# Optimization experiments

Measured on AMD Instinct MI355X. Metric: run time of the kernel, lower is better.

The kernel has to match this reference:

```python
import jax, jax.numpy as jnp
import numpy as np

T, N = 128, 2048
D_LIN, D_AC, D_IM = 300, 74, 35
H_LIN, H_AC, H_IM = 88, 48, 88
TOT_H = H_LIN + H_AC + H_IM          # 224
ATT_IN = 2 * TOT_H                   # 448 (window_dim=2)
MEM = 128
GAMMA_IN = ATT_IN + MEM              # 576
FINAL = TOT_H + MEM                  # 352
OUT_DIM = 1


def _lin(x, w, b):
    # torch nn.Linear: y = x @ W^T + b, W: [out, in]
    return x @ w.T + b


def _lstm_cell(x, h, c, w_ih, w_hh, b_ih, b_hh):
    # torch nn.LSTMCell gate order: i, f, g, o
    gates = x @ w_ih.T + b_ih + h @ w_hh.T + b_hh
    i, f, g, o = jnp.split(gates, 4, axis=-1)
    c2 = jax.nn.sigmoid(f) * c + jax.nn.sigmoid(i) * jnp.tanh(g)
    h2 = jax.nn.sigmoid(o) * jnp.tanh(c2)
    return h2, c2


def _forward(x_lin, x_ac, x_im, p):
    (W_ih_lin, W_hh_lin, b_ih_lin, b_hh_lin,
     W_ih_ac, W_hh_ac, b_ih_ac, b_hh_ac,
     W_ih_im, W_hh_im, b_ih_im, b_hh_im,
     att1_w1, att1_b1, att1_w2, att1_b2,
     att2_w1, att2_b1, att2_w2, att2_b2,
     g1_w1, g1_b1, g1_w2, g1_b2,
     g2_w1, g2_b1, g2_w2, g2_b2,
     out_w1, out_b1, out_w2, out_b2) = p
    n = x_lin.shape[1]
    z = lambda d: jnp.zeros((n, d), dtype=x_lin.dtype)
    init = (z(H_LIN), z(H_LIN), z(H_AC), z(H_AC), z(H_IM), z(H_IM), z(MEM))

    def step(carry, xs):
        h_l, c_l, h_a, c_a, h_i, c_i, mem = carry
        xl, xa, xi = xs
        nh_l, nc_l = _lstm_cell(xl, h_l, c_l, W_ih_lin, W_hh_lin, b_ih_lin, b_hh_lin)
        nh_a, nc_a = _lstm_cell(xa, h_a, c_a, W_ih_ac, W_hh_ac, b_ih_ac, b_hh_ac)
        nh_i, nc_i = _lstm_cell(xi, h_i, c_i, W_ih_im, W_hh_im, b_ih_im, b_hh_im)
        prev_cs = jnp.concatenate([c_l, c_a, c_i], axis=1)
        new_cs = jnp.concatenate([nc_l, nc_a, nc_i], axis=1)
        c_star = jnp.concatenate([prev_cs, new_cs], axis=1)   # [n, 448]
        attn = jax.nn.softmax(
            _lin(jax.nn.relu(_lin(c_star, att1_w1, att1_b1)), att1_w2, att1_b2), axis=1)
        attended = attn * c_star
        c_hat = jnp.tanh(
            _lin(jax.nn.relu(_lin(attended, att2_w1, att2_b1)), att2_w2, att2_b2))
        both = jnp.concatenate([attended, mem], axis=1)       # [n, 576]
        gamma1 = jax.nn.sigmoid(_lin(jax.nn.relu(_lin(both, g1_w1, g1_b1)), g1_w2, g1_b2))
        gamma2 = jax.nn.sigmoid(_lin(jax.nn.relu(_lin(both, g2_w1, g2_b1)), g2_w2, g2_b2))
        new_mem = gamma1 * mem + gamma2 * c_hat
        return ((nh_l, nc_l, nh_a, nc_a, nh_i, nc_i, new_mem),
                (nh_l, nh_a, nh_i, new_mem))

    _, (hs_l, hs_a, hs_i, mems) = jax.lax.scan(step, init, (x_lin, x_ac, x_im))
    feats = jnp.concatenate([hs_l, hs_a, hs_i, mems], axis=-1)  # [T, n, 352]
    out = _lin(jax.nn.relu(_lin(feats, out_w1, out_b1)), out_w2, out_b2)  # [T, n, 1]
    return jnp.transpose(out, (1, 0, 2))  # [n, T, 1] (torch cats over dim=1)


def setup_inputs() -> dict:
    key = jax.random.key(0)
    ks = iter(jax.random.split(key, 64))

    def rn(shape, s=0.05):
        return (jax.random.normal(next(ks), shape) * s).astype(jnp.float32)

    inp = {
        'x_linguistic': rn((T, N, D_LIN), 1.0),
        'x_acoustic': rn((T, N, D_AC), 1.0),
        'x_image': rn((T, N, D_IM), 1.0),
    }
    for name, din, h in [('lin', D_LIN, H_LIN), ('ac', D_AC, H_AC), ('im', D_IM, H_IM)]:
        inp[f'W_ih_{name}'] = rn((4 * h, din))
        inp[f'W_hh_{name}'] = rn((4 * h, h))
        inp[f'b_ih_{name}'] = rn((4 * h,))
        inp[f'b_hh_{name}'] = rn((4 * h,))
    for nm, hdim, din, dout in [('att1', 128, ATT_IN, ATT_IN),
                                ('att2', 256, ATT_IN, MEM),
                                ('g1', 64, GAMMA_IN, MEM),
                                ('g2', 64, GAMMA_IN, MEM),
                                ('out', 64, FINAL, OUT_DIM)]:
        inp[f'{nm}_w1'] = rn((hdim, din))
        inp[f'{nm}_b1'] = rn((hdim,))
        inp[f'{nm}_w2'] = rn((dout, hdim))
        inp[f'{nm}_b2'] = rn((dout,))
    return inp


def reference(x_linguistic, x_acoustic, x_image,
              W_ih_lin, W_hh_lin, b_ih_lin, b_hh_lin,
              W_ih_ac, W_hh_ac, b_ih_ac, b_hh_ac,
              W_ih_im, W_hh_im, b_ih_im, b_hh_im,
              att1_w1, att1_b1, att1_w2, att1_b2,
              att2_w1, att2_b1, att2_w2, att2_b2,
              g1_w1, g1_b1, g1_w2, g1_b2,
              g2_w1, g2_b1, g2_w2, g2_b2,
              out_w1, out_b1, out_w2, out_b2):
    p = (W_ih_lin, W_hh_lin, b_ih_lin, b_hh_lin,
         W_ih_ac, W_hh_ac, b_ih_ac, b_hh_ac,
         W_ih_im, W_hh_im, b_ih_im, b_hh_im,
         att1_w1, att1_b1, att1_w2, att1_b2,
         att2_w1, att2_b1, att2_w2, att2_b2,
         g1_w1, g1_b1, g1_w2, g1_b2,
         g2_w1, g2_b1, g2_w2, g2_b2,
         out_w1, out_b1, out_w2, out_b2)
    return _forward(x_linguistic, x_acoustic, x_image, p)
```

## Files before the change

kernel.cpp:

```cpp
#include <hip/hip_runtime.h>


#define T_STEPS 128

typedef __attribute__((ext_vector_type(8))) short bf16x8;
typedef __attribute__((ext_vector_type(4))) float f32x4;
typedef __attribute__((ext_vector_type(2))) unsigned long long ull2;

#define MFMA_B16(a,b,c) __builtin_amdgcn_mfma_f32_16x16x32_bf16((a),(b),(c),0,0,0)

__device__ __forceinline__ unsigned short f2b(float v) {
  union { float f; unsigned u; } x; x.f = v;
  unsigned r = x.u + 0x7fffu + ((x.u >> 16) & 1u);
  return (unsigned short)(r >> 16);
}
__device__ __forceinline__ float b2f(unsigned short u) {
  union { unsigned u; float f; } x; x.u = ((unsigned)u) << 16; return x.f;
}
__device__ __forceinline__ float sigm(float x){ return 1.0f/(1.0f + __expf(-x)); }
__device__ __forceinline__ float tanh_(float x){ return 1.0f - 2.0f/(1.0f + __expf(2.0f*x)); }

#define OFF_XL     0
#define OFF_XA     10496
#define OFF_XI     13824
#define OFF_CSTAR  16128
#define OFF_ATT    30720
#define OFF_HID    45312
#define OFF_G1H    53760
#define OFF_G2H    56064
#define OFF_FEATS  58368
#define OFF_BIAS   69888
#define OFF_XP     79368
#define LDS_BYTES  110344

#define BG_LIN 0
#define BG_AC  384
#define BG_IM  576
#define B_A1H  960
#define B_LOG  1088
#define B_A2H  1536
#define B_CHAT 1792
#define B_G1H  1920
#define B_G2H  1984
#define B_GM1  2048
#define B_GM2  2176
#define B_OUTH 2304
#define B_OUT2 2368
#define N_BIAS 2369

#define N_TILES 1718
#define PACK_BYTES ((size_t)N_TILES * 1024)
#define XP_ELEMS ((size_t)262144 * 960)
#define XP_BYTES (XP_ELEMS * 2)

#define LA(off,st,row,kk)  (*(const bf16x8*)(lds + (off) + ((((row)*(st)) + (kk)) << 1)))
#define LB(tile)           (*(const bf16x8*)(packc + (((size_t)(tile)) << 10) + (lane << 4)))
#define STB(off,st,row,col,v) (*(unsigned short*)(lds + (off) + ((((row)*(st)) + (col)) << 1)) = f2b(v))
#define LDB(off,st,row,col)   b2f(*(const unsigned short*)(lds + (off) + ((((row)*(st)) + (col)) << 1)))

struct PP { const float* p[35]; };

__device__ __forceinline__ void vmw(int n) {
  switch (n) {
    case 0:  asm volatile("s_waitcnt vmcnt(0)");  break;
    case 1:  asm volatile("s_waitcnt vmcnt(1)");  break;
    case 2:  asm volatile("s_waitcnt vmcnt(2)");  break;
    case 3:  asm volatile("s_waitcnt vmcnt(3)");  break;
    case 4:  asm volatile("s_waitcnt vmcnt(4)");  break;
    case 5:  asm volatile("s_waitcnt vmcnt(5)");  break;
    case 6:  asm volatile("s_waitcnt vmcnt(6)");  break;
    case 7:  asm volatile("s_waitcnt vmcnt(7)");  break;
    case 8:  asm volatile("s_waitcnt vmcnt(8)");  break;
    case 9:  asm volatile("s_waitcnt vmcnt(9)");  break;
    case 10: asm volatile("s_waitcnt vmcnt(10)"); break;
    case 11: asm volatile("s_waitcnt vmcnt(11)"); break;
    case 12: asm volatile("s_waitcnt vmcnt(12)"); break;
    case 13: asm volatile("s_waitcnt vmcnt(13)"); break;
    case 14: asm volatile("s_waitcnt vmcnt(14)"); break;
    default: asm volatile("s_waitcnt vmcnt(15)"); break;
  }
  __builtin_amdgcn_sched_barrier(0);
}

#define ISSUE_B(dst, tile)                                                   \
  { unsigned off_ = (((unsigned)(tile)) << 10) + ((unsigned)lane << 4);      \
    asm volatile("global_load_dwordx4 %0, %1, %2"                            \
                 : "=v"(dst) : "v"(off_), "s"(packc)); }

template<int NTT, class FT, class FB>
__device__ __forceinline__ void reg_loop(const char* packc, int lane,
                                         FT&& tile_of, FB&& body)
{
  constexpr int D = (NTT < 16) ? NTT : 16;
  bf16x8 b[16];
  #pragma unroll
  for (int i = 0; i < D; ++i) ISSUE_B(b[i], tile_of(i));
  #pragma unroll
  for (int i = 0; i < NTT; ++i) {
    vmw((NTT-1-i) < 15 ? (NTT-1-i) : 15);
    body(i, b[i & 15]);
    __builtin_amdgcn_sched_barrier(0);
    if (i + 16 < NTT) ISSUE_B(b[i & 15], tile_of(i + 16));
  }
}

__device__ __forceinline__ float gate_src(const float* Wih, const float* Whh,
                                          int H, int din, int nksx, int col, int k)
{
  int blk = col >> 6, gate = (col >> 4) & 3, u = col & 15;
  int unit = blk*16 + u;
  if (unit >= H) return 0.f;
  int row = gate*H + unit;
  int xk = nksx*32;
  if (k < xk) return (k < din) ? Wih[row*din + k] : 0.f;
  int kk = k - xk;
  return (kk < H) ? Whh[row*H + kk] : 0.f;
}
__device__ __forceinline__ float gate_h(const float* Whh, int H, int col, int k)
{
  int blk = col >> 6, gate = (col >> 4) & 3, u = col & 15;
  int unit = blk*16 + u;
  if (unit >= H || k >= H) return 0.f;
  return Whh[(gate*H + unit)*H + k];
}
__device__ __forceinline__ float gate_x(const float* Wih, int H, int din, int col, int k)
{
  int blk = col >> 6, gate = (col >> 4) & 3, u = col & 15;
  int unit = blk*16 + u;
  if (unit >= H || k >= din) return 0.f;
  return Wih[(gate*H + unit)*din + k];
}
__device__ __forceinline__ float plain_src(const float* W, int nout, int kdim, int col, int k)
{
  return (col < nout && k < kdim) ? W[col*kdim + k] : 0.f;
}

__global__ __launch_bounds__(256) void pack_kernel(PP P, unsigned short* __restrict__ pack,
                                                   float* __restrict__ bias)
{
  int tid = blockIdx.x*blockDim.x + threadIdx.x;
  int wv = tid >> 6, lane = tid & 63;
  int nw = (gridDim.x*blockDim.x) >> 6;
  int c = lane & 15, kg = lane >> 4;

  for (int tile = wv; tile < N_TILES; tile += nw) {
    unsigned short* dst = pack + ((size_t)tile << 9) + lane*8;
    #pragma unroll
    for (int i = 0; i < 8; ++i) {
      int r = tile; int nt, ks; float v; int kk;
      if (r < 312)       { nt=r/13; ks=r-nt*13; kk=ks*32+kg*8+i; v = gate_src(P.p[3], P.p[4], 88,300,10, nt*16+c, kk); }
      else if (r < 372)  { r-=312; nt=r/5;  ks=r-nt*5;  kk=ks*32+kg*8+i; v = gate_src(P.p[7], P.p[8], 48, 74, 3, nt*16+c, kk); }
      else if (r < 492)  { r-=372; nt=r/5;  ks=r-nt*5;  kk=ks*32+kg*8+i; v = gate_src(P.p[11],P.p[12],88, 35, 2, nt*16+c, kk); }
      else if (r < 604)  { r-=492; nt=r/14; ks=r-nt*14; kk=ks*32+kg*8+i; v = plain_src(P.p[15],128,448, nt*16+c, kk); }
      else if (r < 716)  { r-=604; nt=r/4;  ks=r-nt*4;  kk=ks*32+kg*8+i; v = plain_src(P.p[17],448,128, nt*16+c, kk); }
      else if (r < 940)  { r-=716; nt=r/14; ks=r-nt*14; kk=ks*32+kg*8+i; v = plain_src(P.p[19],256,448, nt*16+c, kk); }
      else if (r < 1004) { r-=940; nt=r/8;  ks=r-nt*8;  kk=ks*32+kg*8+i; v = plain_src(P.p[21],128,256, nt*16+c, kk); }
      else if (r < 1076) { r-=1004; nt=r/18; ks=r-nt*18; kk=ks*32+kg*8+i; v = plain_src(P.p[23], 64,576, nt*16+c, kk); }
      else if (r < 1148) { r-=1076; nt=r/18; ks=r-nt*18; kk=ks*32+kg*8+i; v = plain_src(P.p[27], 64,576, nt*16+c, kk); }
      else if (r < 1164) { r-=1148; nt=r/2;  ks=r-nt*2;  kk=ks*32+kg*8+i; v = plain_src(P.p[25],128, 64, nt*16+c, kk); }
      else if (r < 1180) { r-=1164; nt=r/2;  ks=r-nt*2;  kk=ks*32+kg*8+i; v = plain_src(P.p[29],128, 64, nt*16+c, kk); }
      else if (r < 1224) { r-=1180; nt=r/11; ks=r-nt*11; kk=ks*32+kg*8+i; v = plain_src(P.p[31], 64,352, nt*16+c, kk); }
      else if (r < 1226) { r-=1224; ks=r;    kk=ks*32+kg*8+i; v = plain_src(P.p[33],  1, 64, c, kk); }
      else if (r < 1298) { r-=1226; nt=r/3;  ks=r-nt*3;  kk=ks*32+kg*8+i; v = gate_h(P.p[4], 88, nt*16+c, kk); }
      else if (r < 1322) { r-=1298; nt=r/2;  ks=r-nt*2;  kk=ks*32+kg*8+i; v = gate_h(P.p[8], 48, nt*16+c, kk); }
      else if (r < 1394) { r-=1322; nt=r/3;  ks=r-nt*3;  kk=ks*32+kg*8+i; v = gate_h(P.p[12],88, nt*16+c, kk); }
      else if (r < 1634) { r-=1394; nt=r/10; ks=r-nt*10; kk=ks*32+kg*8+i; v = gate_x(P.p[3], 88,300, nt*16+c, kk); }
      else if (r < 1670) { r-=1634; nt=r/3;  ks=r-nt*3;  kk=ks*32+kg*8+i; v = gate_x(P.p[7], 48, 74, nt*16+c, kk); }
      else               { r-=1670; nt=r/2;  ks=r-nt*2;  kk=ks*32+kg*8+i; v = gate_x(P.p[11],88, 35, nt*16+c, kk); }
      dst[i] = f2b(v);
    }
  }

  int NT = gridDim.x*blockDim.x;
  for (int b = tid; b < N_BIAS; b += NT) {
    float v; int r = b;
    if (r < 384)       { int blk=r>>6, g=(r>>4)&3, u=r&15, un=blk*16+u; v = (un<88) ? P.p[5][g*88+un] + P.p[6][g*88+un]  : 0.f; }
    else if (r < 576)  { r-=384; int blk=r>>6, g=(r>>4)&3, u=r&15, un=blk*16+u; v = (un<48) ? P.p[9][g*48+un] + P.p[10][g*48+un] : 0.f; }
    else if (r < 960)  { r-=576; int blk=r>>6, g=(r>>4)&3, u=r&15, un=blk*16+u; v = (un<88) ? P.p[13][g*88+un]+ P.p[14][g*88+un] : 0.f; }
    else if (r < 1088) v = P.p[16][r-960];
    else if (r < 1536) v = P.p[18][r-1088];
    else if (r < 1792) v = P.p[20][r-1536];
    else if (r < 1920) v = P.p[22][r-1792];
    else if (r < 1984) v = P.p[24][r-1920];
    else if (r < 2048) v = P.p[28][r-1984];
    else if (r < 2176) v = P.p[26][r-2048];
    else if (r < 2304) v = P.p[30][r-2176];
    else if (r < 2368) v = P.p[32][r-2304];
    else               v = P.p[34][0];
    bias[b] = v;
  }
}

__global__ __launch_bounds__(1024) void xproj_kernel(
    const float* __restrict__ xlin, const float* __restrict__ xac,
    const float* __restrict__ xim, const unsigned short* __restrict__ pack,
    unsigned short* __restrict__ xp)
{
  __shared__ alignas(16) char slds[81920];
  const char* packc = (const char*)pack;
  const int tid = threadIdx.x, lane = tid & 63, w = tid >> 6;
  const int rA = lane & 15, gA = lane >> 4;
  const int mt = w & 7, half = w >> 3;
  const size_t m0 = (size_t)blockIdx.x * 128;
  const int mr = mt * 16;

  for (int p = tid; p < 9600; p += 1024) {
    int row = p/75, d = p - row*75;
    float4 v = *(const float4*)(xlin + (m0+row)*300 + d*4);
    unsigned long long u = (unsigned long long)f2b(v.x)
      | ((unsigned long long)f2b(v.y) << 16)
      | ((unsigned long long)f2b(v.z) << 32)
      | ((unsigned long long)f2b(v.w) << 48);
    *(unsigned long long*)(slds + (((size_t)row*320 + d*4) << 1)) = u;
  }
  for (int p = tid; p < 1280; p += 1024) {
    int row = p/10, cc = 300 + 2*(p - row*10);
    *(unsigned*)(slds + (((size_t)row*320 + cc) << 1)) = 0;
  }
  __syncthreads();
  for (int blk = half*3; blk < half*3 + 3; ++blk) {
    #pragma unroll
    for (int q = 0; q < 4; ++q) {
      f32x4 acc = {0.f,0.f,0.f,0.f};
      int nt = blk*4 + q;
      bf16x8 a = *(const bf16x8*)(slds + ((((mr+rA)*320) + gA*8) << 1));
      reg_loop<10>(packc, lane,
        [&](int i){ return 1394 + nt*10 + i; },
        [&](int i, bf16x8 bv){
          acc = MFMA_B16(a, bv, acc);
          if (i + 1 < 10) a = *(const bf16x8*)(slds + ((((mr+rA)*320) + (i+1)*32 + gA*8) << 1));
        });
      #pragma unroll
      for (int j = 0; j < 4; ++j)
        xp[(m0 + mr + gA*4 + j)*960 + blk*64 + q*16 + rA] = f2b(acc[j]);
    }
  }
  __syncthreads();

  for (int p = tid; p < 4736; p += 1024) {
    int row = p/37, d = p - row*37;
    float2 v = *(const float2*)(xac + (m0+row)*74 + d*2);
    unsigned uu = (unsigned)f2b(v.x) | ((unsigned)f2b(v.y) << 16);
    *(unsigned*)(slds + (((size_t)row*96 + d*2) << 1)) = uu;
  }
  for (int p = tid; p < 1408; p += 1024) {
    int row = p/11, cc = 74 + 2*(p - row*11);
    *(unsigned*)(slds + (((size_t)row*96 + cc) << 1)) = 0;
  }
  __syncthreads();
  if (half == 0) {
    for (int blk = 0; blk < 3; ++blk) {
      #pragma unroll
      for (int q = 0; q < 4; ++q) {
        f32x4 acc = {0.f,0.f,0.f,0.f};
        int nt = blk*4 + q;
        bf16x8 a = *(const bf16x8*)(slds + ((((mr+rA)*96) + gA*8) << 1));
        reg_loop<3>(packc, lane,
          [&](int i){ return 1634 + nt*3 + i; },
          [&](int i, bf16x8 bv){
            acc = MFMA_B16(a, bv, acc);
            if (i + 1 < 3) a = *(const bf16x8*)(slds + ((((mr+rA)*96) + (i+1)*32 + gA*8) << 1));
          });
        #pragma unroll
        for (int j = 0; j < 4; ++j)
          xp[(m0 + mr + gA*4 + j)*960 + 384 + blk*64 + q*16 + rA] = f2b(acc[j]);
      }
    }
  }
  __syncthreads();

  for (int p = tid; p < 4480; p += 1024) {
    int row = p/35, d = p - row*35;
    *(unsigned short*)(slds + (((size_t)row*64 + d) << 1)) = f2b(xim[(m0+row)*35 + d]);
  }
  for (int p = tid; p < 3712; p += 1024) {
    int row = p/29, cc = 35 + (p - row*29);
    *(unsigned short*)(slds + (((size_t)row*64 + cc) << 1)) = 0;
  }
  __syncthreads();
  if (half == 1) {
    for (int blk = 0; blk < 6; ++blk) {
      #pragma unroll
      for (int q = 0; q < 4; ++q) {
        f32x4 acc = {0.f,0.f,0.f,0.f};
        int nt = blk*4 + q;
        bf16x8 a = *(const bf16x8*)(slds + ((((mr+rA)*64) + gA*8) << 1));
        reg_loop<2>(packc, lane,
          [&](int i){ return 1670 + nt*2 + i; },
          [&](int i, bf16x8 bv){
            acc = MFMA_B16(a, bv, acc);
            if (i + 1 < 2) a = *(const bf16x8*)(slds + ((((mr+rA)*64) + 32 + gA*8) << 1));
          });
        #pragma unroll
        for (int j = 0; j < 4; ++j)
          xp[(m0 + mr + gA*4 + j)*960 + 576 + blk*64 + q*16 + rA] = f2b(acc[j]);
      }
    }
  }
}

template<int NA,int NB>
__device__ __forceinline__ void twin_gate(f32x4 aA[4], f32x4 aB[4], const char* lds,
    const char* packc, int lane, int rA, int gA,
    int tbA, int hsA, int tbB, int hsB)
{
  bf16x8 a;
  reg_loop<(NA+NB)*4>(packc, lane,
    [&](int i){
      if (i < NA*4) { int j = i;        return tbA + (j&3)*NA + (j>>2); }
      else          { int j = i - NA*4; return tbB + (j&3)*NB + (j>>2); }
    },
    [&](int i, bf16x8 bv){
      if (i < NA*4) {
        int q = i & 3, s = i >> 2;
        if (q == 0) a = LA(OFF_FEATS,360, rA, hsA + s*32 + gA*8);
        aA[q] = MFMA_B16(a, bv, aA[q]);
      } else {
        int j = i - NA*4, q = j & 3, s = j >> 2;
        if (q == 0) a = LA(OFF_FEATS,360, rA, hsB + s*32 + gA*8);
        aB[q] = MFMA_B16(a, bv, aB[q]);
      }
    });
}

template<int NKS>
__device__ __forceinline__ void gate_reg_h(f32x4 acc[4], const char* lds, const char* packc,
    int lane, int rA, int gA, int hsec, int tb)
{
  bf16x8 a;
  reg_loop<NKS*4>(packc, lane,
    [&](int i){ return tb + (i & 3)*NKS + (i >> 2); },
    [&](int i, bf16x8 bv){
      int q = i & 3, s = i >> 2;
      if (q == 0) a = LA(OFF_FEATS, 360, rA, hsec + s*32 + gA*8);
      acc[q] = MFMA_B16(a, bv, acc[q]);
    });
}

__global__ __launch_bounds__(512, 2) void fused_kernel(
    const unsigned short* __restrict__ pack, const float* __restrict__ biasg,
    const unsigned short* __restrict__ xp, float* __restrict__ out)
{
  __shared__ alignas(16) char lds[LDS_BYTES];
  const char* packc = (const char*)pack;
  const int tid  = threadIdx.x;
  const int lane = tid & 63;
  const int w    = tid >> 6;
  const int rA   = lane & 15;
  const int gA   = lane >> 4;
  const int n0   = blockIdx.x * 16;
  float* biasLds = (float*)(lds + OFF_BIAS);

  for (int i = tid; i < (OFF_BIAS >> 2); i += 512) ((int*)lds)[i] = 0;
  __syncthreads();
  for (int i = tid; i < N_BIAS; i += 512) biasLds[i] = biasg[i];
  {
    const size_t base0 = ((size_t)n0) * 960;
    for (int q = tid; q < 1920; q += 512) {
      int row = q/120, ch = q - row*120;
      ull2 v = __builtin_nontemporal_load((const ull2*)(xp + base0 + (size_t)row*960 + ch*8));
      *(ull2*)(lds + OFF_XP + (((size_t)row*968 + ch*8) << 1)) = v;
    }
  }
  __syncthreads();

  float cstA[4] = {}, cstB[4] = {};
  float mreg[4] = {};

  int tbA, hsA, cbA, HA, blkA;
  if (w < 6)      { tbA = 1226 + w*12; hsA = 0;  cbA = w*64;  HA = 88; blkA = w; }
  else if (w==6)  { tbA = 1298;        hsA = 88; cbA = 384;   HA = 48; blkA = 0; }
  else            { tbA = 1306;        hsA = 88; cbA = 448;   HA = 48; blkA = 1; }
  int tbB, hsB, cbB, HB, blkB;
  if (w == 0)     { tbB = 1314;            hsB = 88;  cbB = 512;          HB = 48; blkB = 2; }
  else            { tbB = 1322 + (w-1)*12; hsB = 136; cbB = 576+(w-1)*64; HB = 88; blkB = w-1; }

  for (int t = 0; t < T_STEPS; ++t) {
    f32x4 gaccA[4], gaccB[4];
    {
      #pragma unroll
      for (int q = 0; q < 4; ++q) {
        float bvA = biasLds[cbA + q*16 + rA];
        #pragma unroll
        for (int j = 0; j < 4; ++j) {
          int row = gA*4 + j;
          gaccA[q][j] = bvA + b2f(*(const unsigned short*)(lds + OFF_XP + (((size_t)row*968 + cbA + q*16 + rA) << 1)));
        }
        if (w < 7) {
          float bvB = biasLds[cbB + q*16 + rA];
          #pragma unroll
          for (int j = 0; j < 4; ++j) {
            int row = gA*4 + j;
            gaccB[q][j] = bvB + b2f(*(const unsigned short*)(lds + OFF_XP + (((size_t)row*968 + cbB + q*16 + rA) << 1)));
          }
        }
      }
      if (w == 0)      twin_gate<3,2>(gaccA, gaccB, lds, packc, lane, rA, gA, tbA, hsA, tbB, hsB);
      else if (w < 6)  twin_gate<3,3>(gaccA, gaccB, lds, packc, lane, rA, gA, tbA, hsA, tbB, hsB);
      else if (w == 6) twin_gate<2,3>(gaccA, gaccB, lds, packc, lane, rA, gA, tbA, hsA, tbB, hsB);
      else {
        gate_reg_h<2>(gaccA, lds, packc, lane, rA, gA, hsA, tbA);
        if (t > 0) {
          float bv = biasLds[B_OUT2];
          f32x4 oa0 = {bv,bv,bv,bv};
          bf16x8 as[2], bs[2];
          #pragma unroll
          for (int s = 0; s < 2; ++s) { bs[s] = LB(1224 + s); as[s] = LA(OFF_HID,72, rA, s*32+gA*8); }
          #pragma unroll
          for (int s = 0; s < 2; ++s) oa0 = MFMA_B16(as[s], bs[s], oa0);
          if (rA == 0) {
            #pragma unroll
            for (int j = 0; j < 4; ++j)
              __builtin_nontemporal_store(oa0[j], &out[(size_t)(n0 + gA*4 + j)*T_STEPS + (t-1)]);
          }
        }
      }
    }
    __syncthreads();

    {
      int unitA = blkA*16 + rA;
      if (unitA < HA) {
        #pragma unroll
        for (int j = 0; j < 4; ++j) {
          float iv = sigm (gaccA[0][j]);
          float fv = sigm (gaccA[1][j]);
          float gv = tanh_(gaccA[2][j]);
          float ov = sigm (gaccA[3][j]);
          float cp = cstA[j];
          float cn = fv*cp + iv*gv;
          float hn = ov*tanh_(cn);
          cstA[j] = cn;
          int row = gA*4 + j;
          STB(OFF_CSTAR,456, row, hsA + unitA,        cp);
          STB(OFF_CSTAR,456, row, 224 + hsA + unitA,  cn);
          STB(OFF_FEATS,360, row, hsA + unitA,        hn);
        }
      }
      if (w < 7) {
        int unitB = blkB*16 + rA;
        if (unitB < HB) {
          #pragma unroll
          for (int j = 0; j < 4; ++j) {
            float iv = sigm (gaccB[0][j]);
            float fv = sigm (gaccB[1][j]);
            float gv = tanh_(gaccB[2][j]);
            float ov = sigm (gaccB[3][j]);
            float cp = cstB[j];
            float cn = fv*cp + iv*gv;
            float hn = ov*tanh_(cn);
            cstB[j] = cn;
            int row = gA*4 + j;
            STB(OFF_CSTAR,456, row, hsB + unitB,        cp);
            STB(OFF_CSTAR,456, row, 224 + hsB + unitB,  cn);
            STB(OFF_FEATS,360, row, hsB + unitB,        hn);
          }
        }
      }
    }
    __syncthreads();

    {
      int n = w;
      float bv = biasLds[B_A1H + n*16 + rA];
      f32x4 a0v = {bv,bv,bv,bv};
      bf16x8 a = LA(OFF_CSTAR,456, rA, gA*8);
      reg_loop<14>(packc, lane,
        [&](int i){ return 492 + n*14 + i; },
        [&](int i, bf16x8 bv8){
          a0v = MFMA_B16(a, bv8, a0v);
          if (i + 1 < 14) a = LA(OFF_CSTAR,456, rA, (i+1)*32+gA*8);
        });
      #pragma unroll
      for (int j = 0; j < 4; ++j)
        STB(OFF_HID,136, gA*4 + j, n*16 + rA, fmaxf(a0v[j], 0.f));
    }
    __syncthreads();

    {
      bf16x8 a4[4];
      #pragma unroll
      for (int s = 0; s < 4; ++s) a4[s] = LA(OFF_HID,136, rA, s*32+gA*8);
      f32x4 l[4];
      #pragma unroll
      for (int k = 0; k < 4; ++k) {
        float bv = biasLds[B_LOG + (w + 8*k)*16 + rA];
        l[k] = (f32x4){bv,bv,bv,bv};
      }
      if (w < 4) {
        reg_loop<16>(packc, lane,
          [&](int i){ return 604 + (w + 8*(i>>2))*4 + (i&3); },
          [&](int i, bf16x8 bv8){ l[i>>2] = MFMA_B16(a4[i&3], bv8, l[i>>2]); });
        #pragma unroll
        for (int k = 0; k < 4; ++k)
          #pragma unroll
          for (int j = 0; j < 4; ++j)
            STB(OFF_ATT,456, gA*4 + j, (w + 8*k)*16 + rA, l[k][j]);
      } else {
        reg_loop<12>(packc, lane,
          [&](int i){ return 604 + (w + 8*(i>>2))*4 + (i&3); },
          [&](int i, bf16x8 bv8){ l[i>>2] = MFMA_B16(a4[i&3], bv8, l[i>>2]); });
        #pragma unroll
        for (int k = 0; k < 3; ++k)
          #pragma unroll
          for (int j = 0; j < 4; ++j)
            STB(OFF_ATT,456, gA*4 + j, (w + 8*k)*16 + rA, l[k][j]);
      }
    }
    __syncthreads();

    {
      ull2 xr[4];
      const bool do_stage = (t < T_STEPS-1);
      const size_t base = ((size_t)(t+1)*2048 + n0)*960;
      if (do_stage) {
        #pragma unroll
        for (int k = 0; k < 4; ++k) {
          int q = tid + k*512;
          if (q < 1920) {
            int row = q/120, ch = q - row*120;
            xr[k] = __builtin_nontemporal_load((const ull2*)(xp + base + (size_t)row*960 + ch*8));
          }
        }
      }
      int row = w*2 + (lane >> 5);
      int cb  = lane & 31;
      float v[14];
      float mx = -3.0e38f;
      #pragma unroll
      for (int q = 0; q < 14; ++q) { v[q] = LDB(OFF_ATT,456,row, cb + 32*q); mx = fmaxf(mx, v[q]); }
      #pragma unroll
      for (int mk = 1; mk < 32; mk <<= 1) mx = fmaxf(mx, __shfl_xor(mx, mk));
      float sm = 0.f;
      #pragma unroll
      for (int q = 0; q < 14; ++q) { v[q] = __expf(v[q] - mx); sm += v[q]; }
      #pragma unroll
      for (int mk = 1; mk < 32; mk <<= 1) sm += __shfl_xor(sm, mk);
      float inv = 1.0f / sm;
      #pragma unroll
      for (int q = 0; q < 14; ++q) {
        int c = cb + 32*q;
        float cs = LDB(OFF_CSTAR,456,row,c);
        STB(OFF_ATT,456,row,c, v[q]*inv*cs);
      }
      if (do_stage) {
        asm volatile("s_waitcnt vmcnt(0)");
        __builtin_amdgcn_sched_barrier(0);
        #pragma unroll
        for (int k = 0; k < 4; ++k) {
          int q = tid + k*512;
          if (q < 1920) {
            int row2 = q/120, ch = q - row2*120;
            *(ull2*)(lds + OFF_XP + (((size_t)row2*968 + ch*8) << 1)) = xr[k];
          }
        }
      }
    }
    __syncthreads();

    {
      int nb = w*2;
      int which = w >> 2, n = w & 3;
      int tbq = which ? 1076 : 1004;
      int bb  = which ? B_G2H : B_G1H;
      int oo  = which ? OFF_G2H : OFF_G1H;
      float b0 = biasLds[B_A2H + nb*16 + rA];
      float b1 = biasLds[B_A2H + (nb+1)*16 + rA];
      float bg = biasLds[bb + n*16 + rA];
      f32x4 A0 = {b0,b0,b0,b0}, A1 = {b1,b1,b1,b1}, G = {bg,bg,bg,bg};
      reg_loop<46>(packc, lane,
        [&](int i){
          if (i < 14) return 716 + nb*14 + i;
          if (i < 28) return 716 + (nb+1)*14 + (i-14);
          return tbq + n*18 + (i-28);
        },
        [&](int i, bf16x8 bv8){
          if (i < 14) {
            bf16x8 a = LA(OFF_ATT,456, rA, i*32+gA*8);
            A0 = MFMA_B16(a, bv8, A0);
          } else if (i < 28) {
            int s = i - 14;
            bf16x8 a = LA(OFF_ATT,456, rA, s*32+gA*8);
            A1 = MFMA_B16(a, bv8, A1);
          } else {
            int s = i - 28;
            bf16x8 a = (s < 14) ? LA(OFF_ATT,456, rA, s*32+gA*8)
                                : LA(OFF_FEATS,360, rA, 224 + (s-14)*32 + gA*8);
            G = MFMA_B16(a, bv8, G);
          }
        });
      #pragma unroll
      for (int j = 0; j < 4; ++j) {
        STB(OFF_HID,264, gA*4 + j, nb*16 + rA,     fmaxf(A0[j], 0.f));
        STB(OFF_HID,264, gA*4 + j, (nb+1)*16 + rA, fmaxf(A1[j], 0.f));
        STB(oo,72,       gA*4 + j, n*16 + rA,      fmaxf(G[j],  0.f));
      }
    }
    __syncthreads();

    {
      int n = w;
      float bc = biasLds[B_CHAT + n*16 + rA];
      float b1 = biasLds[B_GM1  + n*16 + rA];
      float b2 = biasLds[B_GM2  + n*16 + rA];
      f32x4 cc0={bc,bc,bc,bc};
      f32x4 g10={b1,b1,b1,b1};
      f32x4 g20={b2,b2,b2,b2};
      bf16x8 a = LA(OFF_HID,264, rA, gA*8);
      reg_loop<12>(packc, lane,
        [&](int i){
          if (i < 8)  return 940 + n*8 + i;
          if (i < 10) return 1148 + n*2 + (i - 8);
          return 1164 + n*2 + (i - 10);
        },
        [&](int i, bf16x8 bv8){
          if (i < 8)       cc0 = MFMA_B16(a, bv8, cc0);
          else if (i < 10) g10 = MFMA_B16(a, bv8, g10);
          else             g20 = MFMA_B16(a, bv8, g20);
          if (i + 1 < 8)        a = LA(OFF_HID,264, rA, (i+1)*32+gA*8);
          else if (i + 1 == 8)  a = LA(OFF_G1H,72, rA, gA*8);
          else if (i + 1 == 9)  a = LA(OFF_G1H,72, rA, 32+gA*8);
          else if (i + 1 == 10) a = LA(OFF_G2H,72, rA, gA*8);
          else if (i + 1 == 11) a = LA(OFF_G2H,72, rA, 32+gA*8);
        });
      #pragma unroll
      for (int j = 0; j < 4; ++j) {
        float ch = tanh_(cc0[j]), ga = sigm(g10[j]), gb = sigm(g20[j]);
        float mn = ga*mreg[j] + gb*ch;
        mreg[j] = mn;
        STB(OFF_FEATS,360, gA*4 + j, 224 + n*16 + rA, mn);
      }
    }
    __syncthreads();

    if (w < 4) {
      int n = w;
      float bv = biasLds[B_OUTH + n*16 + rA];
      f32x4 a0v = {bv,bv,bv,bv};
      bf16x8 a = LA(OFF_FEATS,360, rA, gA*8);
      reg_loop<11>(packc, lane,
        [&](int i){ return 1180 + n*11 + i; },
        [&](int i, bf16x8 bv8){
          a0v = MFMA_B16(a, bv8, a0v);
          if (i + 1 < 11) a = LA(OFF_FEATS,360, rA, (i+1)*32+gA*8);
        });
      #pragma unroll
      for (int j = 0; j < 4; ++j)
        STB(OFF_HID,72, gA*4 + j, n*16 + rA, fmaxf(a0v[j], 0.f));
    }
    __syncthreads();
  }

  if (w == 7) {
    float bv = biasLds[B_OUT2];
    f32x4 oa0 = {bv,bv,bv,bv};
    bf16x8 as[2], bs[2];
    #pragma unroll
    for (int s = 0; s < 2; ++s) { bs[s] = LB(1224 + s); as[s] = LA(OFF_HID,72, rA, s*32+gA*8); }
    #pragma unroll
    for (int s = 0; s < 2; ++s) oa0 = MFMA_B16(as[s], bs[s], oa0);
    if (rA == 0) {
      #pragma unroll
      for (int j = 0; j < 4; ++j)
        __builtin_nontemporal_store(oa0[j], &out[(size_t)(n0 + gA*4 + j)*T_STEPS + 127]);
    }
  }
}

extern "C" void kernel_launch(void* const* d_in, const int* in_sizes, int n_in,
                              void* d_out, int out_size, void* d_ws, size_t ws_size,
                              hipStream_t stream) {
  (void)in_sizes; (void)n_in; (void)out_size; (void)ws_size;
  PP P;
  for (int i = 0; i < 35; ++i) P.p[i] = (const float*)d_in[i];
  unsigned short* pack = (unsigned short*)d_ws;
  float* bias = (float*)((char*)d_ws + PACK_BYTES);
  unsigned short* xp = (unsigned short*)((char*)d_ws + PACK_BYTES + 16384);

  hipLaunchKernelGGL(pack_kernel, dim3(320), dim3(256), 0, stream, P, pack, bias);
  hipLaunchKernelGGL(xproj_kernel, dim3(2048), dim3(1024), 0, stream,
                     P.p[0], P.p[1], P.p[2], pack, xp);
  hipLaunchKernelGGL(fused_kernel, dim3(128), dim3(512), 0, stream,
                     pack, bias, xp, (float*)d_out);
}
```

Measured before the change: 4.691 ms.

## Replace rolling 16-deep weight prefetch with double-buffered 8-tile chunks

The register prefetch loop for packed weight tiles changes from a rolling window of up to 16 outstanding global loads, each waited on individually, to double-buffered chunks of 8. The next chunk is issued and then waited on as a group before the current chunk's MFMAs run. LDS A-operand loads move inside each MFMA body instead of being software-prefetched one step ahead, leaving the compiler to schedule them. This cuts the number of fine-grained vmcnt waits and the register pressure, at the cost of less load-latency hiding per tile and possible stalls on LDS reads.

```diff
diff --git a/kernel.cpp b/kernel.cpp
--- a/kernel.cpp
+++ b/kernel.cpp
@@ -70,14 +70,7 @@
     case 5:  asm volatile("s_waitcnt vmcnt(5)");  break;
     case 6:  asm volatile("s_waitcnt vmcnt(6)");  break;
     case 7:  asm volatile("s_waitcnt vmcnt(7)");  break;
-    case 8:  asm volatile("s_waitcnt vmcnt(8)");  break;
-    case 9:  asm volatile("s_waitcnt vmcnt(9)");  break;
-    case 10: asm volatile("s_waitcnt vmcnt(10)"); break;
-    case 11: asm volatile("s_waitcnt vmcnt(11)"); break;
-    case 12: asm volatile("s_waitcnt vmcnt(12)"); break;
-    case 13: asm volatile("s_waitcnt vmcnt(13)"); break;
-    case 14: asm volatile("s_waitcnt vmcnt(14)"); break;
-    default: asm volatile("s_waitcnt vmcnt(15)"); break;
+    default: asm volatile("s_waitcnt vmcnt(8)");  break;
   }
   __builtin_amdgcn_sched_barrier(0);
 }
@@ -91,16 +84,26 @@
 __device__ __forceinline__ void reg_loop(const char* packc, int lane,
                                          FT&& tile_of, FB&& body)
 {
-  constexpr int D = (NTT < 16) ? NTT : 16;
-  bf16x8 b[16];
+  constexpr int NC = (NTT + 7) >> 3;
+  bf16x8 b[2][8];
   #pragma unroll
-  for (int i = 0; i < D; ++i) ISSUE_B(b[i], tile_of(i));
+  for (int j = 0; j < 8; ++j) if (j < NTT) ISSUE_B(b[0][j], tile_of(j));
   #pragma unroll
-  for (int i = 0; i < NTT; ++i) {
-    vmw((NTT-1-i) < 15 ? (NTT-1-i) : 15);
-    body(i, b[i & 15]);
+  for (int c = 0; c < NC; ++c) {
+    const int base = c * 8;
+    const int cnt  = (NTT - base < 8) ? (NTT - base) : 8;
+    const int nbase = base + 8;
+    const int ncnt  = (NTT - nbase < 8) ? (NTT - nbase) : ((NTT - nbase < 0) ? 0 : 8);
+    if (nbase < NTT) {
+      #pragma unroll
+      for (int j = 0; j < 8; ++j) if (j < ncnt) ISSUE_B(b[(c+1)&1][j], tile_of(nbase + j));
+      vmw(ncnt);
+    } else {
+      vmw(0);
+    }
+    #pragma unroll
+    for (int j = 0; j < 8; ++j) if (j < cnt) body(base + j, b[c&1][j]);
     __builtin_amdgcn_sched_barrier(0);
-    if (i + 16 < NTT) ISSUE_B(b[i & 15], tile_of(i + 16));
   }
 }
 
@@ -223,12 +226,11 @@
     for (int q = 0; q < 4; ++q) {
       f32x4 acc = {0.f,0.f,0.f,0.f};
       int nt = blk*4 + q;
-      bf16x8 a = *(const bf16x8*)(slds + ((((mr+rA)*320) + gA*8) << 1));
       reg_loop<10>(packc, lane,
         [&](int i){ return 1394 + nt*10 + i; },
         [&](int i, bf16x8 bv){
+          bf16x8 a = *(const bf16x8*)(slds + ((((mr+rA)*320) + i*32 + gA*8) << 1));
           acc = MFMA_B16(a, bv, acc);
-          if (i + 1 < 10) a = *(const bf16x8*)(slds + ((((mr+rA)*320) + (i+1)*32 + gA*8) << 1));
         });
       #pragma unroll
       for (int j = 0; j < 4; ++j)
@@ -254,12 +256,11 @@
       for (int q = 0; q < 4; ++q) {
         f32x4 acc = {0.f,0.f,0.f,0.f};
         int nt = blk*4 + q;
-        bf16x8 a = *(const bf16x8*)(slds + ((((mr+rA)*96) + gA*8) << 1));
         reg_loop<3>(packc, lane,
           [&](int i){ return 1634 + nt*3 + i; },
           [&](int i, bf16x8 bv){
+            bf16x8 a = *(const bf16x8*)(slds + ((((mr+rA)*96) + i*32 + gA*8) << 1));
             acc = MFMA_B16(a, bv, acc);
-            if (i + 1 < 3) a = *(const bf16x8*)(slds + ((((mr+rA)*96) + (i+1)*32 + gA*8) << 1));
           });
         #pragma unroll
         for (int j = 0; j < 4; ++j)
@@ -284,12 +285,11 @@
       for (int q = 0; q < 4; ++q) {
         f32x4 acc = {0.f,0.f,0.f,0.f};
         int nt = blk*4 + q;
-        bf16x8 a = *(const bf16x8*)(slds + ((((mr+rA)*64) + gA*8) << 1));
         reg_loop<2>(packc, lane,
           [&](int i){ return 1670 + nt*2 + i; },
           [&](int i, bf16x8 bv){
+            bf16x8 a = *(const bf16x8*)(slds + ((((mr+rA)*64) + i*32 + gA*8) << 1));
             acc = MFMA_B16(a, bv, acc);
-            if (i + 1 < 2) a = *(const bf16x8*)(slds + ((((mr+rA)*64) + 32 + gA*8) << 1));
           });
         #pragma unroll
         for (int j = 0; j < 4; ++j)
@@ -304,7 +304,6 @@
     const char* packc, int lane, int rA, int gA,
     int tbA, int hsA, int tbB, int hsB)
 {
-  bf16x8 a;
   reg_loop<(NA+NB)*4>(packc, lane,
     [&](int i){
       if (i < NA*4) { int j = i;        return tbA + (j&3)*NA + (j>>2); }
@@ -313,11 +312,11 @@
     [&](int i, bf16x8 bv){
       if (i < NA*4) {
         int q = i & 3, s = i >> 2;
-        if (q == 0) a = LA(OFF_FEATS,360, rA, hsA + s*32 + gA*8);
+        bf16x8 a = LA(OFF_FEATS,360, rA, hsA + s*32 + gA*8);
         aA[q] = MFMA_B16(a, bv, aA[q]);
       } else {
         int j = i - NA*4, q = j & 3, s = j >> 2;
-        if (q == 0) a = LA(OFF_FEATS,360, rA, hsB + s*32 + gA*8);
+        bf16x8 a = LA(OFF_FEATS,360, rA, hsB + s*32 + gA*8);
         aB[q] = MFMA_B16(a, bv, aB[q]);
       }
     });
@@ -327,12 +326,11 @@
 __device__ __forceinline__ void gate_reg_h(f32x4 acc[4], const char* lds, const char* packc,
     int lane, int rA, int gA, int hsec, int tb)
 {
-  bf16x8 a;
   reg_loop<NKS*4>(packc, lane,
     [&](int i){ return tb + (i & 3)*NKS + (i >> 2); },
     [&](int i, bf16x8 bv){
       int q = i & 3, s = i >> 2;
-      if (q == 0) a = LA(OFF_FEATS, 360, rA, hsec + s*32 + gA*8);
+      bf16x8 a = LA(OFF_FEATS, 360, rA, hsec + s*32 + gA*8);
       acc[q] = MFMA_B16(a, bv, acc[q]);
     });
 }
@@ -464,12 +462,11 @@
       int n = w;
       float bv = biasLds[B_A1H + n*16 + rA];
       f32x4 a0v = {bv,bv,bv,bv};
-      bf16x8 a = LA(OFF_CSTAR,456, rA, gA*8);
       reg_loop<14>(packc, lane,
         [&](int i){ return 492 + n*14 + i; },
         [&](int i, bf16x8 bv8){
+          bf16x8 a = LA(OFF_CSTAR,456, rA, i*32+gA*8);
           a0v = MFMA_B16(a, bv8, a0v);
-          if (i + 1 < 14) a = LA(OFF_CSTAR,456, rA, (i+1)*32+gA*8);
         });
       #pragma unroll
       for (int j = 0; j < 4; ++j)
@@ -478,9 +475,6 @@
     __syncthreads();
 
     {
-      bf16x8 a4[4];
-      #pragma unroll
-      for (int s = 0; s < 4; ++s) a4[s] = LA(OFF_HID,136, rA, s*32+gA*8);
       f32x4 l[4];
       #pragma unroll
       for (int k = 0; k < 4; ++k) {
@@ -490,7 +484,10 @@
       if (w < 4) {
         reg_loop<16>(packc, lane,
           [&](int i){ return 604 + (w + 8*(i>>2))*4 + (i&3); },
-          [&](int i, bf16x8 bv8){ l[i>>2] = MFMA_B16(a4[i&3], bv8, l[i>>2]); });
+          [&](int i, bf16x8 bv8){
+            bf16x8 a = LA(OFF_HID,136, rA, (i&3)*32+gA*8);
+            l[i>>2] = MFMA_B16(a, bv8, l[i>>2]);
+          });
         #pragma unroll
         for (int k = 0; k < 4; ++k)
           #pragma unroll
@@ -499,7 +496,10 @@
       } else {
         reg_loop<12>(packc, lane,
           [&](int i){ return 604 + (w + 8*(i>>2))*4 + (i&3); },
-          [&](int i, bf16x8 bv8){ l[i>>2] = MFMA_B16(a4[i&3], bv8, l[i>>2]); });
+          [&](int i, bf16x8 bv8){
+            bf16x8 a = LA(OFF_HID,136, rA, (i&3)*32+gA*8);
+            l[i>>2] = MFMA_B16(a, bv8, l[i>>2]);
+          });
         #pragma unroll
         for (int k = 0; k < 3; ++k)
           #pragma unroll
@@ -606,7 +606,6 @@
       f32x4 cc0={bc,bc,bc,bc};
       f32x4 g10={b1,b1,b1,b1};
       f32x4 g20={b2,b2,b2,b2};
-      bf16x8 a = LA(OFF_HID,264, rA, gA*8);
       reg_loop<12>(packc, lane,
         [&](int i){
           if (i < 8)  return 940 + n*8 + i;
@@ -614,14 +613,16 @@
           return 1164 + n*2 + (i - 10);
         },
         [&](int i, bf16x8 bv8){
-          if (i < 8)       cc0 = MFMA_B16(a, bv8, cc0);
-          else if (i < 10) g10 = MFMA_B16(a, bv8, g10);
-          else             g20 = MFMA_B16(a, bv8, g20);
-          if (i + 1 < 8)        a = LA(OFF_HID,264, rA, (i+1)*32+gA*8);
-          else if (i + 1 == 8)  a = LA(OFF_G1H,72, rA, gA*8);
-          else if (i + 1 == 9)  a = LA(OFF_G1H,72, rA, 32+gA*8);
-          else if (i + 1 == 10) a = LA(OFF_G2H,72, rA, gA*8);
-          else if (i + 1 == 11) a = LA(OFF_G2H,72, rA, 32+gA*8);
+          if (i < 8) {
+            bf16x8 a = LA(OFF_HID,264, rA, i*32+gA*8);
+            cc0 = MFMA_B16(a, bv8, cc0);
+          } else if (i < 10) {
+            bf16x8 a = LA(OFF_G1H,72, rA, (i-8)*32+gA*8);
+            g10 = MFMA_B16(a, bv8, g10);
+          } else {
+            bf16x8 a = LA(OFF_G2H,72, rA, (i-10)*32+gA*8);
+            g20 = MFMA_B16(a, bv8, g20);
+          }
         });
       #pragma unroll
       for (int j = 0; j < 4; ++j) {
@@ -637,12 +638,11 @@
       int n = w;
       float bv = biasLds[B_OUTH + n*16 + rA];
       f32x4 a0v = {bv,bv,bv,bv};
-      bf16x8 a = LA(OFF_FEATS,360, rA, gA*8);
       reg_loop<11>(packc, lane,
         [&](int i){ return 1180 + n*11 + i; },
         [&](int i, bf16x8 bv8){
+          bf16x8 a = LA(OFF_FEATS,360, rA, i*32+gA*8);
           a0v = MFMA_B16(a, bv8, a0v);
-          if (i + 1 < 11) a = LA(OFF_FEATS,360, rA, (i+1)*32+gA*8);
         });
       #pragma unroll
       for (int j = 0; j < 4; ++j)
```

Measured after the change: 5.975 ms. 27.4% more time.
